# Optimization experiments

Measured on AMD Instinct MI355X. Metric: run time of the kernel, lower is better.

The kernel has to match this reference:

```python
import jax, jax.numpy as jnp
import numpy as np
from jax import lax

H = 256  # hidden_size


def _conv1d(x, w, b):
    # x: (N, Cin, L), w: (Cout, Cin, K) -> (N, Cout, L-K+1), VALID, stride 1
    y = lax.conv_general_dilated(x, w, window_strides=(1,), padding='VALID',
                                 dimension_numbers=('NCH', 'OIH', 'NCH'))
    return y + b[None, :, None]


def _gru_dir(x, Wih, Whh, bih, bhh):
    # x: (L, N, H). Torch GRU cell equations.
    L, N, _ = x.shape
    gi = jnp.einsum('lnh,gh->lng', x, Wih) + bih  # (L, N, 3H) precomputed input gates
    h0 = jnp.zeros((N, H), x.dtype)

    def step(h, gi_t):
        gh = h @ Whh.T + bhh                       # (N, 3H)
        ir, iz, inn = jnp.split(gi_t, 3, axis=-1)
        hr, hz, hn = jnp.split(gh, 3, axis=-1)
        r = jax.nn.sigmoid(ir + hr)
        z = jax.nn.sigmoid(iz + hz)
        n = jnp.tanh(inn + r * hn)
        h_new = (1.0 - z) * n + z * h
        return h_new, h_new

    hT, ys = lax.scan(step, h0, gi)
    return ys, hT  # (L, N, H), (N, H)


def setup_inputs() -> dict:
    key = jax.random.key(0)
    ks = jax.random.split(key, 14)
    N, C, L = 32, 13, 4096
    s = 0.1
    inp = {
        'X': jax.random.normal(ks[0], (N, C, L), jnp.float32),
        'W1': jax.random.normal(ks[1], (H // 2, C, 3), jnp.float32) * s,
        'b1': jax.random.normal(ks[2], (H // 2,), jnp.float32) * s,
        'W2': jax.random.normal(ks[3], (H, H // 2, 3), jnp.float32) * s,
        'b2': jax.random.normal(ks[4], (H,), jnp.float32) * s,
        'Wih_f': jax.random.normal(ks[5], (3 * H, H), jnp.float32) * s,
        'Whh_f': jax.random.normal(ks[6], (3 * H, H), jnp.float32) * s,
        'bih_f': jax.random.normal(ks[7], (3 * H,), jnp.float32) * s,
        'bhh_f': jax.random.normal(ks[8], (3 * H,), jnp.float32) * s,
        'Wih_b': jax.random.normal(ks[9], (3 * H, H), jnp.float32) * s,
        'Whh_b': jax.random.normal(ks[10], (3 * H, H), jnp.float32) * s,
        'bih_b': jax.random.normal(ks[11], (3 * H,), jnp.float32) * s,
        'bhh_b': jax.random.normal(ks[12], (3 * H,), jnp.float32) * s,
    }
    return inp


def reference(X, W1, b1, W2, b2, Wih_f, Whh_f, bih_f, bhh_f,
              Wih_b, Whh_b, bih_b, bhh_b):
    # dropouts are identity in eval mode; N>1 so squeeze() is a no-op
    x = _conv1d(X, W1, b1)           # (N, H/2, L-2)
    x = _conv1d(x, W2, b2)           # (N, H,   L-4)
    x = x[:, :, ::2]                 # MaxPool1d(kernel=1, stride=2) == stride-2 subsample
    x = jnp.transpose(x, (2, 0, 1))  # (L', N, H)

    out_f, hT_f = _gru_dir(x, Wih_f, Whh_f, bih_f, bhh_f)
    # backward direction: reverse time, scan, reverse outputs
    out_b_rev, hT_b = _gru_dir(x[::-1], Wih_b, Whh_b, bih_b, bhh_b)
    out_b = out_b_rev[::-1]

    # original: fwd + flip(bwd along FEATURE axis), averaged, ReLU (faithful to np.flip(axis=-1))
    comb = jax.nn.relu((out_f + out_b[:, :, ::-1]) * 0.5)  # (L', N, H)
    hidden_last = hT_b[None]                                # hidden[-1].unsqueeze(0): (1, N, H)
    return comb, hidden_last
```

## Files before the change

### kernel.cpp

```cpp
#include <hip/hip_runtime.h>
#include <hip/hip_fp16.h>
#include <cstdint>
#include <cstddef>

#define L_SEQ 2046
#define NBATCH 32
#define HID 256
#define M_PAD 65536

typedef _Float16 h2vec __attribute__((ext_vector_type(2)));

static __device__ __forceinline__ uint32_t pack2(float a, float b) {
  __half2 h = __floats2half2_rn(a, b);
  return __builtin_bit_cast(uint32_t, h);
}

static __device__ __forceinline__ float fdot2u(uint32_t w, uint32_t h, float c) {
#if __has_builtin(__builtin_amdgcn_fdot2)
  return __builtin_amdgcn_fdot2(__builtin_bit_cast(h2vec, w),
                                __builtin_bit_cast(h2vec, h), c, false);
#else
  __half2 a = __builtin_bit_cast(__half2, w);
  __half2 b = __builtin_bit_cast(__half2, h);
  float2 fa = __half22float2(a), fb = __half22float2(b);
  return c + fa.x * fb.x + fa.y * fb.y;
#endif
}

__global__ void k_conv_im2col(const float* __restrict__ X,
                              const float* __restrict__ W1,
                              const float* __restrict__ b1,
                              __half* __restrict__ A1h) {
  int j   = threadIdx.x;
  int row = blockIdx.x;
  int l2 = row >> 5, n = row & 31;
  float v = 0.f;
  if (l2 < L_SEQ) {
    int ci = j / 3;
    int k  = j - 3 * ci;
    int p  = 2 * l2 + k;
    const float* xb = X + (size_t)n * 13 * 4096 + p;
    const float* w  = W1 + ci * 39;
    float acc = b1[ci];
#pragma unroll
    for (int c = 0; c < 13; c++) {
      const float* xp = xb + (size_t)c * 4096;
      acc += xp[0] * w[3*c+0] + xp[1] * w[3*c+1] + xp[2] * w[3*c+2];
    }
    v = acc;
  }
  A1h[(size_t)row * 384 + j] = __float2half(v);
}

__global__ __launch_bounds__(256, 4) void k_gemm_h(
    const __half* __restrict__ A, const float* __restrict__ B,
    const float* __restrict__ bias, __half* __restrict__ C,
    int K, int ldC, int col_off) {
  __shared__ float As[32][132];
  __shared__ float Bs[32][132];
  const int tid = threadIdx.x;
  const int m_blk = blockIdx.x * 128;
  const int n_blk = blockIdx.y * 128;
  const int tx = tid & 15, ty = tid >> 4;
  const int m0 = tx * 8, n0 = ty * 8;
  const int sr = tid >> 3;
  const int sc = 4 * (tid & 7);
  const int ar = tid >> 1;
  const int ak = 16 * (tid & 1);

  float acc[8][8];
#pragma unroll
  for (int i = 0; i < 8; i++)
#pragma unroll
    for (int j = 0; j < 8; j++) acc[i][j] = 0.f;

  for (int kc = 0; kc < K; kc += 32) {
    const __half* ap = A + (size_t)(m_blk + ar) * K + kc + ak;
    uint4 h0 = *(const uint4*)(ap);
    uint4 h1 = *(const uint4*)(ap + 8);
    {
      uint32_t hw[8] = {h0.x, h0.y, h0.z, h0.w, h1.x, h1.y, h1.z, h1.w};
#pragma unroll
      for (int p = 0; p < 8; p++) {
        float2 f = __half22float2(__builtin_bit_cast(__half2, hw[p]));
        As[ak + 2*p    ][ar] = f.x;
        As[ak + 2*p + 1][ar] = f.y;
      }
    }
#pragma unroll
    for (int i = 0; i < 4; i++) {
      int r = i * 32 + sr;
      float4 vb = *(const float4*)(B + (size_t)(n_blk + r) * K + kc + sc);
      Bs[sc+0][r] = vb.x; Bs[sc+1][r] = vb.y; Bs[sc+2][r] = vb.z; Bs[sc+3][r] = vb.w;
    }
    __syncthreads();
#pragma unroll 8
    for (int k = 0; k < 32; k++) {
      float a[8], b[8];
      *(float4*)(a)     = *(const float4*)&As[k][m0];
      *(float4*)(a + 4) = *(const float4*)&As[k][m0 + 4];
      *(float4*)(b)     = *(const float4*)&Bs[k][n0];
      *(float4*)(b + 4) = *(const float4*)&Bs[k][n0 + 4];
#pragma unroll
      for (int i = 0; i < 8; i++)
#pragma unroll
        for (int j = 0; j < 8; j++) acc[i][j] += a[i] * b[j];
    }
    __syncthreads();
  }
  float bj[8];
#pragma unroll
  for (int j = 0; j < 8; j++) bj[j] = bias[n_blk + n0 + j];
#pragma unroll
  for (int i = 0; i < 8; i++) {
    uint4 o;
    o.x = pack2(acc[i][0] + bj[0], acc[i][1] + bj[1]);
    o.y = pack2(acc[i][2] + bj[2], acc[i][3] + bj[3]);
    o.z = pack2(acc[i][4] + bj[4], acc[i][5] + bj[5]);
    o.w = pack2(acc[i][6] + bj[6], acc[i][7] + bj[7]);
    *(uint4*)(C + (size_t)(m_blk + m0 + i) * ldC + col_off + n_blk + n0) = o;
  }
}

__global__ void k_packw(const float* __restrict__ Whh_f,
                        const float* __restrict__ Whh_b,
                        uint4* __restrict__ Wpk) {
  int idx = blockIdx.x * 256 + threadIdx.x;
  int d   = idx / 24576;
  int r   = idx - d * 24576;
  int jq  = r >> 9;
  int tid = r & 511;
  int q   = jq / 3, gt = jq - 3 * q;
  int lane = tid & 63, wave = tid >> 6;
  int kh = lane & 1, g = wave * 32 + (lane >> 1);
  const float* W = d ? Whh_b : Whh_f;
  const float* src = W + (size_t)(gt * 256 + g) * 256 + kh * 128 + 8 * q;
  uint4 o;
  o.x = pack2(src[0], src[1]);
  o.y = pack2(src[2], src[3]);
  o.z = pack2(src[4], src[5]);
  o.w = pack2(src[6], src[7]);
  Wpk[(size_t)idx] = o;
}

__global__ __attribute__((amdgpu_flat_work_group_size(512, 512),
                          amdgpu_waves_per_eu(2, 2)))
void k_gru(
    const __half* __restrict__ gih, const uint4* __restrict__ Wpk,
    const float* __restrict__ bhh_f, const float* __restrict__ bhh_b,
    float* __restrict__ outF, __half* __restrict__ outBh,
    float* __restrict__ hT) {
  const int blk = blockIdx.x;
  const int dir = blk >> 5;
  const int n   = blk & 31;
  const int tid = threadIdx.x;
  const int lane = tid & 63;
  const int kh  = lane & 1;
  const int g   = (tid >> 6) * 32 + (lane >> 1);

  const float* bhh = dir ? bhh_b : bhh_f;

  uint4 wv[48];
  {
    const uint4* wp = Wpk + (size_t)dir * 24576 + tid;
#pragma unroll
    for (int j = 0; j < 48; j++) wv[j] = wp[j * 512];
#pragma unroll
    for (int j = 0; j < 48; j++) {
      asm volatile("" : "+v"(wv[j].x), "+v"(wv[j].y), "+v"(wv[j].z), "+v"(wv[j].w));
    }
  }
  const float bh0 = bhh[g];
  const float bh1 = bhh[256 + g];
  const float bh2 = bhh[512 + g];

  __shared__ __align__(16) __half hs[2][256];
  if (tid < 128) ((uint32_t*)hs)[tid] = 0u;
  float hp = 0.f;

  const __half* gr = gih + ((size_t)(dir ? (size_t)(L_SEQ - 1) * NBATCH : 0) + n) * 1536
                         + dir * 768 + g;
  const ptrdiff_t gstep = dir ? -(ptrdiff_t)(NBATCH * 1536) : (ptrdiff_t)(NBATCH * 1536);
  __half pi0 = __float2half(0.f), pi1 = pi0, pi2 = pi0;
  if (kh == 0) { pi0 = gr[0]; pi1 = gr[256]; pi2 = gr[512]; }
  __syncthreads();

  for (int t = 0; t < L_SEQ; t++) {
    const uint4* hb = (const uint4*)hs[t & 1];
    float a0 = 0.f, a1 = 0.f, a2 = 0.f;
#pragma unroll
    for (int q = 0; q < 16; q++) {
      uint4 hq = hb[q * 2 + kh];
      uint4 u0 = wv[q * 3 + 0];
      uint4 u1 = wv[q * 3 + 1];
      uint4 u2 = wv[q * 3 + 2];
      a0 = fdot2u(u0.x, hq.x, a0);
      a0 = fdot2u(u0.y, hq.y, a0);
      a0 = fdot2u(u0.z, hq.z, a0);
      a0 = fdot2u(u0.w, hq.w, a0);
      a1 = fdot2u(u1.x, hq.x, a1);
      a1 = fdot2u(u1.y, hq.y, a1);
      a1 = fdot2u(u1.z, hq.z, a1);
      a1 = fdot2u(u1.w, hq.w, a1);
      a2 = fdot2u(u2.x, hq.x, a2);
      a2 = fdot2u(u2.y, hq.y, a2);
      a2 = fdot2u(u2.z, hq.z, a2);
      a2 = fdot2u(u2.w, hq.w, a2);
    }
    a0 += __shfl_xor(a0, 1);
    a1 += __shfl_xor(a1, 1);
    a2 += __shfl_xor(a2, 1);

    if (kh == 0) {
      float hr = a0 + bh0;
      float hz = a1 + bh1;
      float hn = a2 + bh2;
      float ir  = __half2float(pi0);
      float iz  = __half2float(pi1);
      float inn = __half2float(pi2);
      float rr = 1.f / (1.f + __expf(-(ir + hr)));
      float zz = 1.f / (1.f + __expf(-(iz + hz)));
      float e  = __expf(2.f * (inn + rr * hn));
      float nn = 1.f - 2.f / (e + 1.f);
      float hnew = (1.f - zz) * nn + zz * hp;
      hp = hnew;
      __half hh = __float2half(hnew);
      int swi = ((g & 127) >> 3) * 16 + (g >> 7) * 8 + (g & 7);
      hs[(t + 1) & 1][swi] = hh;
      const int l = dir ? (L_SEQ - 1 - t) : t;
      uint32_t oi = ((uint32_t)l * NBATCH + n) * HID + g;
      if (dir == 0) outF[oi] = hnew;
      else          outBh[oi] = hh;
      gr += gstep;
      if (t + 1 < L_SEQ) { pi0 = gr[0]; pi1 = gr[256]; pi2 = gr[512]; }
    }
    __syncthreads();
  }
  if (dir == 1 && kh == 0) hT[n * HID + g] = hp;
}

__global__ void k_combine(float* __restrict__ outF,
                          const __half* __restrict__ outBh) {
  int idx = blockIdx.x * 256 + threadIdx.x;
  int c = idx & 255;
  float v = 0.5f * (outF[idx] + __half2float(outBh[idx + 255 - 2 * c]));
  outF[idx] = v > 0.f ? v : 0.f;
}

extern "C" void kernel_launch(void* const* d_in, const int* in_sizes, int n_in,
                              void* d_out, int out_size, void* d_ws, size_t ws_size,
                              hipStream_t stream) {
  const float* X     = (const float*)d_in[0];
  const float* W1    = (const float*)d_in[1];
  const float* b1    = (const float*)d_in[2];
  const float* W2    = (const float*)d_in[3];
  const float* b2    = (const float*)d_in[4];
  const float* Wih_f = (const float*)d_in[5];
  const float* Whh_f = (const float*)d_in[6];
  const float* bih_f = (const float*)d_in[7];
  const float* bhh_f = (const float*)d_in[8];
  const float* Wih_b = (const float*)d_in[9];
  const float* Whh_b = (const float*)d_in[10];
  const float* bih_b = (const float*)d_in[11];
  const float* bhh_b = (const float*)d_in[12];

  char* wsb = (char*)d_ws;
  __half* gih   = (__half*)(wsb);
  __half* A1h   = (__half*)(wsb + 201326592);
  __half* outBh = (__half*)(wsb + 201326592);
  uint4*  Wpk   = (uint4*)(wsb + 234848768);

  float*  outF  = (float*)d_out;
  __half* xsubh = (__half*)d_out;
  float*  hT    = outF + (size_t)L_SEQ * NBATCH * HID;

  k_conv_im2col<<<dim3(M_PAD), 384, 0, stream>>>(X, W1, b1, A1h);
  k_gemm_h<<<dim3(512, 2), 256, 0, stream>>>(A1h, W2, b2, xsubh, 384, 256, 0);
  k_packw<<<dim3(192), 256, 0, stream>>>(Whh_f, Whh_b, Wpk);
  k_gemm_h<<<dim3(512, 6), 256, 0, stream>>>(xsubh, Wih_f, bih_f, gih, 256, 1536, 0);
  k_gemm_h<<<dim3(512, 6), 256, 0, stream>>>(xsubh, Wih_b, bih_b, gih, 256, 1536, 768);
  k_gru<<<dim3(64), 512, 0, stream>>>(gih, Wpk, bhh_f, bhh_b, outF, outBh, hT);
  k_combine<<<dim3(65472), 256, 0, stream>>>(outF, outBh);
}
```

Before: 3.684 ms.

## Replace scalar FP32 GEMM with MFMA fp16 GEMM using direct global-to-LDS loads

The SIMT FP32 outer-product GEMM used for conv2 and the GRU input-gate projections is replaced by a kernel built on 16x16x32 f16 MFMA instructions. Tiles are staged into XOR-swizzled LDS with global_load_lds. Weights are first converted to fp16 by small new kernels into workspace buffers, so B operands are rounded to half precision. The epilogue now writes scalar half values per lane instead of packed 16-byte rows, which may reduce store coalescing. The change also depends on the extra workspace beyond the previous layout being available.

```diff
diff --git a/kernel.cpp b/kernel.cpp
--- a/kernel.cpp
+++ b/kernel.cpp
@@ -8,7 +8,9 @@
 #define HID 256
 #define M_PAD 65536
 
-typedef _Float16 h2vec __attribute__((ext_vector_type(2)));
+typedef _Float16 h2vec  __attribute__((ext_vector_type(2)));
+typedef _Float16 half8v __attribute__((ext_vector_type(8)));
+typedef float    f32x4  __attribute__((ext_vector_type(4)));
 
 static __device__ __forceinline__ uint32_t pack2(float a, float b) {
   __half2 h = __floats2half2_rn(a, b);
@@ -25,6 +27,12 @@
   float2 fa = __half22float2(a), fb = __half22float2(b);
   return c + fa.x * fb.x + fa.y * fb.y;
 #endif
+}
+
+static __device__ __forceinline__ void gload_lds16(const void* g, void* l) {
+  __builtin_amdgcn_global_load_lds(
+      (const __attribute__((address_space(1))) void*)g,
+      (__attribute__((address_space(3))) void*)l, 16, 0, 0);
 }
 
 __global__ void k_conv_im2col(const float* __restrict__ X,
@@ -52,73 +60,89 @@
   A1h[(size_t)row * 384 + j] = __float2half(v);
 }
 
-__global__ __launch_bounds__(256, 4) void k_gemm_h(
-    const __half* __restrict__ A, const float* __restrict__ B,
+__global__ void k_cvt_h(const float* __restrict__ src, __half* __restrict__ dst,
+                        int nelem) {
+  int i = blockIdx.x * 256 + threadIdx.x;
+  if (i < nelem) dst[i] = __float2half(src[i]);
+}
+
+__global__ __launch_bounds__(256, 3) void k_gemm_mfma(
+    const __half* __restrict__ A, const __half* __restrict__ Bh,
     const float* __restrict__ bias, __half* __restrict__ C,
     int K, int ldC, int col_off) {
-  __shared__ float As[32][132];
-  __shared__ float Bs[32][132];
-  const int tid = threadIdx.x;
+  __shared__ __half Asl[128 * 64];
+  __shared__ __half Bsl[128 * 64];
+  const int tid  = threadIdx.x;
+  const int wave = tid >> 6, lane = tid & 63;
   const int m_blk = blockIdx.x * 128;
   const int n_blk = blockIdx.y * 128;
-  const int tx = tid & 15, ty = tid >> 4;
-  const int m0 = tx * 8, n0 = ty * 8;
-  const int sr = tid >> 3;
-  const int sc = 4 * (tid & 7);
-  const int ar = tid >> 1;
-  const int ak = 16 * (tid & 1);
-
-  float acc[8][8];
-#pragma unroll
-  for (int i = 0; i < 8; i++)
-#pragma unroll
-    for (int j = 0; j < 8; j++) acc[i][j] = 0.f;
-
-  for (int kc = 0; kc < K; kc += 32) {
-    const __half* ap = A + (size_t)(m_blk + ar) * K + kc + ak;
-    uint4 h0 = *(const uint4*)(ap);
-    uint4 h1 = *(const uint4*)(ap + 8);
-    {
-      uint32_t hw[8] = {h0.x, h0.y, h0.z, h0.w, h1.x, h1.y, h1.z, h1.w};
-#pragma unroll
-      for (int p = 0; p < 8; p++) {
-        float2 f = __half22float2(__builtin_bit_cast(__half2, hw[p]));
-        As[ak + 2*p    ][ar] = f.x;
-        As[ak + 2*p + 1][ar] = f.y;
+  const int wm = wave >> 1, wn = wave & 1;
+
+  f32x4 acc[4][4];
+#pragma unroll
+  for (int i = 0; i < 4; i++)
+#pragma unroll
+    for (int j = 0; j < 4; j++) acc[i][j] = (f32x4)0.f;
+
+  int srow[4], sko[4];
+#pragma unroll
+  for (int i = 0; i < 4; i++) {
+    int s = (i * 4 + wave) * 64 + lane;
+    srow[i] = s >> 3;
+    sko[i]  = (s & 7) ^ ((s >> 3) & 7);
+  }
+
+  for (int kc = 0; kc < K; kc += 64) {
+#pragma unroll
+    for (int i = 0; i < 4; i++) {
+      int s = (i * 4 + wave) * 64 + lane;
+      gload_lds16(A + (size_t)(m_blk + srow[i]) * K + kc + sko[i] * 8,
+                  &Asl[s * 8]);
+    }
+#pragma unroll
+    for (int i = 0; i < 4; i++) {
+      int s = (i * 4 + wave) * 64 + lane;
+      gload_lds16(Bh + (size_t)(n_blk + srow[i]) * K + kc + sko[i] * 8,
+                  &Bsl[s * 8]);
+    }
+    __syncthreads();
+#pragma unroll
+    for (int kb = 0; kb < 2; kb++) {
+      half8v af[4], bf[4];
+#pragma unroll
+      for (int mi = 0; mi < 4; mi++) {
+        int row = wm * 64 + mi * 16 + (lane & 15);
+        int c   = (kb * 4 + (lane >> 4)) ^ (row & 7);
+        af[mi] = *(const half8v*)&Asl[row * 64 + c * 8];
       }
-    }
-#pragma unroll
-    for (int i = 0; i < 4; i++) {
-      int r = i * 32 + sr;
-      float4 vb = *(const float4*)(B + (size_t)(n_blk + r) * K + kc + sc);
-      Bs[sc+0][r] = vb.x; Bs[sc+1][r] = vb.y; Bs[sc+2][r] = vb.z; Bs[sc+3][r] = vb.w;
+#pragma unroll
+      for (int ni = 0; ni < 4; ni++) {
+        int row = wn * 64 + ni * 16 + (lane & 15);
+        int c   = (kb * 4 + (lane >> 4)) ^ (row & 7);
+        bf[ni] = *(const half8v*)&Bsl[row * 64 + c * 8];
+      }
+#pragma unroll
+      for (int mi = 0; mi < 4; mi++)
+#pragma unroll
+        for (int ni = 0; ni < 4; ni++)
+          acc[mi][ni] = __builtin_amdgcn_mfma_f32_16x16x32_f16(
+              af[mi], bf[ni], acc[mi][ni], 0, 0, 0);
     }
     __syncthreads();
-#pragma unroll 8
-    for (int k = 0; k < 32; k++) {
-      float a[8], b[8];
-      *(float4*)(a)     = *(const float4*)&As[k][m0];
-      *(float4*)(a + 4) = *(const float4*)&As[k][m0 + 4];
-      *(float4*)(b)     = *(const float4*)&Bs[k][n0];
-      *(float4*)(b + 4) = *(const float4*)&Bs[k][n0 + 4];
-#pragma unroll
-      for (int i = 0; i < 8; i++)
-#pragma unroll
-        for (int j = 0; j < 8; j++) acc[i][j] += a[i] * b[j];
-    }
-    __syncthreads();
-  }
-  float bj[8];
-#pragma unroll
-  for (int j = 0; j < 8; j++) bj[j] = bias[n_blk + n0 + j];
-#pragma unroll
-  for (int i = 0; i < 8; i++) {
-    uint4 o;
-    o.x = pack2(acc[i][0] + bj[0], acc[i][1] + bj[1]);
-    o.y = pack2(acc[i][2] + bj[2], acc[i][3] + bj[3]);
-    o.z = pack2(acc[i][4] + bj[4], acc[i][5] + bj[5]);
-    o.w = pack2(acc[i][6] + bj[6], acc[i][7] + bj[7]);
-    *(uint4*)(C + (size_t)(m_blk + m0 + i) * ldC + col_off + n_blk + n0) = o;
+  }
+#pragma unroll
+  for (int ni = 0; ni < 4; ni++) {
+    int col = wn * 64 + ni * 16 + (lane & 15);
+    float bj = bias[n_blk + col];
+#pragma unroll
+    for (int mi = 0; mi < 4; mi++) {
+      int row0 = m_blk + wm * 64 + mi * 16 + (lane >> 4) * 4;
+#pragma unroll
+      for (int r = 0; r < 4; r++) {
+        C[(size_t)(row0 + r) * ldC + col_off + n_blk + col] =
+            __float2half(acc[mi][ni][r] + bj);
+      }
+    }
   }
 }
 
@@ -266,19 +290,25 @@
 
   char* wsb = (char*)d_ws;
   __half* gih   = (__half*)(wsb);
+  __half* W2h   = (__half*)(wsb);
   __half* A1h   = (__half*)(wsb + 201326592);
   __half* outBh = (__half*)(wsb + 201326592);
   uint4*  Wpk   = (uint4*)(wsb + 234848768);
+  __half* WihfH = (__half*)(wsb + 235635200);
+  __half* WihbH = (__half*)(wsb + 236028416);
 
   float*  outF  = (float*)d_out;
   __half* xsubh = (__half*)d_out;
   float*  hT    = outF + (size_t)L_SEQ * NBATCH * HID;
 
   k_conv_im2col<<<dim3(M_PAD), 384, 0, stream>>>(X, W1, b1, A1h);
-  k_gemm_h<<<dim3(512, 2), 256, 0, stream>>>(A1h, W2, b2, xsubh, 384, 256, 0);
+  k_cvt_h<<<dim3(384), 256, 0, stream>>>(W2, W2h, 98304);
+  k_gemm_mfma<<<dim3(512, 2), 256, 0, stream>>>(A1h, W2h, b2, xsubh, 384, 256, 0);
+  k_cvt_h<<<dim3(768), 256, 0, stream>>>(Wih_f, WihfH, 196608);
+  k_cvt_h<<<dim3(768), 256, 0, stream>>>(Wih_b, WihbH, 196608);
   k_packw<<<dim3(192), 256, 0, stream>>>(Whh_f, Whh_b, Wpk);
-  k_gemm_h<<<dim3(512, 6), 256, 0, stream>>>(xsubh, Wih_f, bih_f, gih, 256, 1536, 0);
-  k_gemm_h<<<dim3(512, 6), 256, 0, stream>>>(xsubh, Wih_b, bih_b, gih, 256, 1536, 768);
+  k_gemm_mfma<<<dim3(512, 6), 256, 0, stream>>>(xsubh, WihfH, bih_f, gih, 256, 1536, 0);
+  k_gemm_mfma<<<dim3(512, 6), 256, 0, stream>>>(xsubh, WihbH, bih_b, gih, 256, 1536, 768);
   k_gru<<<dim3(64), 512, 0, stream>>>(gih, Wpk, bhh_f, bhh_b, outF, outBh, hT);
   k_combine<<<dim3(65472), 256, 0, stream>>>(outF, outBh);
 }
```

Result: faster. 3.053 ms (-17.1%).
